# Kernel tuning notes

Hardware: AMD Instinct MI355X
Metric: run time of the kernel (lower is better)

The kernel has to match this reference:

```python
import jax, jax.numpy as jnp
import numpy as np

B, T, E, D, H = 8, 64, 4, 256, 1024  # batch, num_tokens, num_experts, hidden_dim, ffn_hidden_dim
SPARSITY_WEIGHT = 0.01


def setup_inputs() -> dict:
    key = jax.random.key(0)
    k_x, k_fc1, k_fc2, k_wr, k_br = jax.random.split(key, 5)
    x = jax.random.normal(k_x, (B, T, D), dtype=jnp.float32)
    # xavier_uniform per (t,e) slice: bound = sqrt(6/(fan_in+fan_out))
    a = float(np.sqrt(6.0 / (D + H)))
    fc1 = jax.random.uniform(k_fc1, (T, E, D, H), minval=-a, maxval=a, dtype=jnp.float32)
    b1 = jnp.zeros((T, E, H), dtype=jnp.float32)
    fc2 = jax.random.uniform(k_fc2, (T, E, H, D), minval=-a, maxval=a, dtype=jnp.float32)
    b2 = jnp.zeros((T, E, D), dtype=jnp.float32)
    # per-token routers (nn.Linear default init: U(-1/sqrt(D), 1/sqrt(D)))
    br_bound = float(1.0 / np.sqrt(D))
    Wr = jax.random.uniform(k_wr, (T, E, D), minval=-br_bound, maxval=br_bound, dtype=jnp.float32)
    br = jax.random.uniform(k_br, (T, E), minval=-br_bound, maxval=br_bound, dtype=jnp.float32)
    return {"x": x, "fc1": fc1, "b1": b1, "fc2": fc2, "b2": b2, "Wr": Wr, "br": br}


def reference(x, fc1, b1, fc2, b2, Wr, br):
    # x: [B,T,D]
    # ReLU routing gates per token/expert: [B,T,E]
    gates = jax.nn.relu(jnp.einsum('btd,ted->bte', x, Wr) + br)
    bsz = x.shape[0]
    aux_loss = SPARSITY_WEIGHT * gates.sum() / (bsz * x.shape[1])
    # Expert FFN, batched over (token, expert): hidden [B,T,E,H]
    hidden = jax.nn.gelu(jnp.einsum('btd,tedh->bteh', x, fc1) + b1, approximate=False)
    # dropout rate is 0.0 -> identity
    expert_out = jnp.einsum('bteh,tehd->bted', hidden, fc2) + b2  # [B,T,E,D]
    output = jnp.sum(expert_out * gates[..., None], axis=2)  # [B,T,D]
    return output, aux_loss
```

## Files before the change

kernel.cpp:

```cpp
#include <hip/hip_runtime.h>
#include <hip/hip_bf16.h>

namespace {

constexpr int kB = 8, kT = 64, kE = 4, kD = 256, kH = 1024;
constexpr int kNC = 4;
constexpr int kHc = kH / kNC;

__device__ __forceinline__ float gelu_exact(float v) {
  return 0.5f * v * (1.0f + erff(v * 0.70710678118654752f));
}

__global__ __launch_bounds__(256, 4)
void moe_ffn_kernel(const float* __restrict__ x,
                    const float* __restrict__ fc1,
                    const float* __restrict__ b1,
                    const float* __restrict__ fc2,
                    const float* __restrict__ b2,
                    const float* __restrict__ Wr,
                    const float* __restrict__ br,
                    float* __restrict__ out) {
  __shared__ float xs[kB][kD];
  __shared__ float hid[kB][kHc];
  __shared__ float gates_s[kB];

  const int tid = threadIdx.x;
  const int bid = blockIdx.x;
  const int te  = bid / kNC;
  const int c   = bid % kNC;
  const int t   = te >> 2;
  const int h0  = c * kHc;

#pragma unroll
  for (int b = 0; b < kB; ++b)
    xs[b][tid] = x[((size_t)b * kT + t) * kD + tid];
  __syncthreads();

  const int wave = tid >> 6, lane = tid & 63;

  {
    const float* __restrict__ wr = Wr + (size_t)te * kD;
    const float w0 = wr[lane], w1 = wr[lane + 64], w2 = wr[lane + 128], w3 = wr[lane + 192];
#pragma unroll
    for (int bb = 0; bb < 2; ++bb) {
      const int b = wave + bb * 4;
      float p = xs[b][lane] * w0 + xs[b][lane + 64] * w1 +
                xs[b][lane + 128] * w2 + xs[b][lane + 192] * w3;
#pragma unroll
      for (int off = 32; off; off >>= 1) p += __shfl_xor(p, off);
      if (lane == 0) {
        const float g = p + br[te];
        gates_s[b] = g > 0.0f ? g : 0.0f;
      }
    }
  }

  {
    const float* __restrict__ w = fc1 + (size_t)te * kD * kH + h0 + tid;
    float acc[kB] = {0.f, 0.f, 0.f, 0.f, 0.f, 0.f, 0.f, 0.f};
#pragma unroll 8
    for (int d = 0; d < kD; ++d) {
      const float wv = w[(size_t)d * kH];
#pragma unroll
      for (int b = 0; b < kB; ++b) acc[b] = fmaf(xs[b][d], wv, acc[b]);
    }
    const float bias = b1[(size_t)te * kH + h0 + tid];
#pragma unroll
    for (int b = 0; b < kB; ++b) hid[b][tid] = gelu_exact(acc[b] + bias);
  }
  __syncthreads();

  {
    const float* __restrict__ w = fc2 + (size_t)te * kH * kD + (size_t)h0 * kD + tid;
    float acc[kB] = {0.f, 0.f, 0.f, 0.f, 0.f, 0.f, 0.f, 0.f};
#pragma unroll 8
    for (int i = 0; i < kHc; ++i) {
      const float wv = w[(size_t)i * kD];
#pragma unroll
      for (int b = 0; b < kB; ++b) acc[b] = fmaf(hid[b][i], wv, acc[b]);
    }
    const float bias2 = (c == 0) ? b2[(size_t)te * kD + tid] : 0.f;
#pragma unroll
    for (int b = 0; b < kB; ++b)
      atomicAdd(&out[((size_t)b * kT + t) * kD + tid], gates_s[b] * (acc[b] + bias2));

    if (c == 0 && tid == 0) {
      float gs = 0.f;
#pragma unroll
      for (int b = 0; b < kB; ++b) gs += gates_s[b];
      atomicAdd(&out[(size_t)kB * kT * kD], 0.01f * gs * (1.0f / (kB * kT)));
    }
  }
}

}

extern "C" void kernel_launch(void* const* d_in, const int* in_sizes, int n_in,
                              void* d_out, int out_size, void* d_ws, size_t ws_size,
                              hipStream_t stream) {
  const float* x   = (const float*)d_in[0];
  const float* fc1 = (const float*)d_in[1];
  const float* b1  = (const float*)d_in[2];
  const float* fc2 = (const float*)d_in[3];
  const float* b2  = (const float*)d_in[4];
  const float* Wr  = (const float*)d_in[5];
  const float* br  = (const float*)d_in[6];
  float* out = (float*)d_out;

  hipMemsetAsync(d_out, 0, (size_t)out_size * sizeof(float), stream);

  moe_ffn_kernel<<<dim3(kT * kE * kNC), dim3(256), 0, stream>>>(x, fc1, b1, fc2, b2, Wr, br, out);
}
```

Baseline: 104.6 us.

## Split reduction dim across waves with float4 weight loads and LDS reduction

```diff
diff --git a/kernel.cpp b/kernel.cpp
--- a/kernel.cpp
+++ b/kernel.cpp
@@ -22,28 +22,35 @@
                     float* __restrict__ out) {
   __shared__ float xs[kB][kD];
   __shared__ float hid[kB][kHc];
+  __shared__ float red[kB][kD];
   __shared__ float gates_s[kB];
 
-  const int tid = threadIdx.x;
-  const int bid = blockIdx.x;
-  const int te  = bid / kNC;
-  const int c   = bid % kNC;
-  const int t   = te >> 2;
-  const int h0  = c * kHc;
-
-#pragma unroll
-  for (int b = 0; b < kB; ++b)
-    xs[b][tid] = x[((size_t)b * kT + t) * kD + tid];
+  const int tid  = threadIdx.x;
+  const int bid  = blockIdx.x;
+  const int te   = bid >> 2;
+  const int c    = bid & 3;
+  const int t    = te >> 2;
+  const int h0   = c * kHc;
+  const int wave = tid >> 6, lane = tid & 63;
+
+  {
+    const float4* __restrict__ xsrc = reinterpret_cast<const float4*>(x);
+    float4* xdst = reinterpret_cast<float4*>(&xs[0][0]);
+#pragma unroll
+    for (int i = 0; i < 2; ++i) {
+      const int f = i * 256 + tid;
+      const int b = f >> 6, d4 = f & 63;
+      xdst[f] = xsrc[(size_t)(b * kT + t) * (kD / 4) + d4];
+    }
+  }
   __syncthreads();
-
-  const int wave = tid >> 6, lane = tid & 63;
 
   {
     const float* __restrict__ wr = Wr + (size_t)te * kD;
     const float w0 = wr[lane], w1 = wr[lane + 64], w2 = wr[lane + 128], w3 = wr[lane + 192];
 #pragma unroll
     for (int bb = 0; bb < 2; ++bb) {
-      const int b = wave + bb * 4;
+      const int b = wave * 2 + bb;
       float p = xs[b][lane] * w0 + xs[b][lane + 64] * w1 +
                 xs[b][lane + 128] * w2 + xs[b][lane + 192] * w3;
 #pragma unroll
@@ -55,34 +62,125 @@
     }
   }
 
-  {
-    const float* __restrict__ w = fc1 + (size_t)te * kD * kH + h0 + tid;
-    float acc[kB] = {0.f, 0.f, 0.f, 0.f, 0.f, 0.f, 0.f, 0.f};
-#pragma unroll 8
-    for (int d = 0; d < kD; ++d) {
-      const float wv = w[(size_t)d * kH];
-#pragma unroll
-      for (int b = 0; b < kB; ++b) acc[b] = fmaf(xs[b][d], wv, acc[b]);
-    }
+  float4 acc[kB];
+#pragma unroll
+  for (int b = 0; b < kB; ++b) acc[b] = make_float4(0.f, 0.f, 0.f, 0.f);
+  {
+    const float4* __restrict__ wp =
+        reinterpret_cast<const float4*>(fc1 + (size_t)te * (kD * kH));
+    const int hq = (h0 >> 2) + lane;
+    const int d0 = wave * 64;
+    for (int dg = 0; dg < 16; ++dg) {
+      const int d = d0 + dg * 4;
+      const float4 wv0 = wp[(size_t)(d + 0) * (kH / 4) + hq];
+      const float4 wv1 = wp[(size_t)(d + 1) * (kH / 4) + hq];
+      const float4 wv2 = wp[(size_t)(d + 2) * (kH / 4) + hq];
+      const float4 wv3 = wp[(size_t)(d + 3) * (kH / 4) + hq];
+#pragma unroll
+      for (int b = 0; b < kB; ++b) {
+        const float4 xv = *reinterpret_cast<const float4*>(&xs[b][d]);
+        acc[b].x = fmaf(xv.x, wv0.x, acc[b].x);
+        acc[b].y = fmaf(xv.x, wv0.y, acc[b].y);
+        acc[b].z = fmaf(xv.x, wv0.z, acc[b].z);
+        acc[b].w = fmaf(xv.x, wv0.w, acc[b].w);
+        acc[b].x = fmaf(xv.y, wv1.x, acc[b].x);
+        acc[b].y = fmaf(xv.y, wv1.y, acc[b].y);
+        acc[b].z = fmaf(xv.y, wv1.z, acc[b].z);
+        acc[b].w = fmaf(xv.y, wv1.w, acc[b].w);
+        acc[b].x = fmaf(xv.z, wv2.x, acc[b].x);
+        acc[b].y = fmaf(xv.z, wv2.y, acc[b].y);
+        acc[b].z = fmaf(xv.z, wv2.z, acc[b].z);
+        acc[b].w = fmaf(xv.z, wv2.w, acc[b].w);
+        acc[b].x = fmaf(xv.w, wv3.x, acc[b].x);
+        acc[b].y = fmaf(xv.w, wv3.y, acc[b].y);
+        acc[b].z = fmaf(xv.w, wv3.z, acc[b].z);
+        acc[b].w = fmaf(xv.w, wv3.w, acc[b].w);
+      }
+    }
+  }
+#pragma unroll
+  for (int g = 0; g < 4; ++g) {
+    if (wave == g) {
+#pragma unroll
+      for (int b = 0; b < kB; ++b) {
+        float4* hp = reinterpret_cast<float4*>(&hid[b][0]) + lane;
+        if (g == 0) {
+          *hp = acc[b];
+        } else {
+          float4 v = *hp;
+          v.x += acc[b].x; v.y += acc[b].y; v.z += acc[b].z; v.w += acc[b].w;
+          *hp = v;
+        }
+      }
+    }
+    __syncthreads();
+  }
+  {
     const float bias = b1[(size_t)te * kH + h0 + tid];
 #pragma unroll
-    for (int b = 0; b < kB; ++b) hid[b][tid] = gelu_exact(acc[b] + bias);
+    for (int b = 0; b < kB; ++b) hid[b][tid] = gelu_exact(hid[b][tid] + bias);
   }
   __syncthreads();
 
-  {
-    const float* __restrict__ w = fc2 + (size_t)te * kH * kD + (size_t)h0 * kD + tid;
-    float acc[kB] = {0.f, 0.f, 0.f, 0.f, 0.f, 0.f, 0.f, 0.f};
-#pragma unroll 8
-    for (int i = 0; i < kHc; ++i) {
-      const float wv = w[(size_t)i * kD];
-#pragma unroll
-      for (int b = 0; b < kB; ++b) acc[b] = fmaf(hid[b][i], wv, acc[b]);
-    }
-    const float bias2 = (c == 0) ? b2[(size_t)te * kD + tid] : 0.f;
+  float4 acc2[kB];
+#pragma unroll
+  for (int b = 0; b < kB; ++b) acc2[b] = make_float4(0.f, 0.f, 0.f, 0.f);
+  {
+    const float4* __restrict__ wp =
+        reinterpret_cast<const float4*>(fc2 + (size_t)te * (kH * kD));
+    const int hb = wave * 64;
+    for (int hg = 0; hg < 16; ++hg) {
+      const int hl = hb + hg * 4;
+      const int h  = h0 + hl;
+      const float4 wv0 = wp[(size_t)(h + 0) * (kD / 4) + lane];
+      const float4 wv1 = wp[(size_t)(h + 1) * (kD / 4) + lane];
+      const float4 wv2 = wp[(size_t)(h + 2) * (kD / 4) + lane];
+      const float4 wv3 = wp[(size_t)(h + 3) * (kD / 4) + lane];
+#pragma unroll
+      for (int b = 0; b < kB; ++b) {
+        const float4 hv = *reinterpret_cast<const float4*>(&hid[b][hl]);
+        acc2[b].x = fmaf(hv.x, wv0.x, acc2[b].x);
+        acc2[b].y = fmaf(hv.x, wv0.y, acc2[b].y);
+        acc2[b].z = fmaf(hv.x, wv0.z, acc2[b].z);
+        acc2[b].w = fmaf(hv.x, wv0.w, acc2[b].w);
+        acc2[b].x = fmaf(hv.y, wv1.x, acc2[b].x);
+        acc2[b].y = fmaf(hv.y, wv1.y, acc2[b].y);
+        acc2[b].z = fmaf(hv.y, wv1.z, acc2[b].z);
+        acc2[b].w = fmaf(hv.y, wv1.w, acc2[b].w);
+        acc2[b].x = fmaf(hv.z, wv2.x, acc2[b].x);
+        acc2[b].y = fmaf(hv.z, wv2.y, acc2[b].y);
+        acc2[b].z = fmaf(hv.z, wv2.z, acc2[b].z);
+        acc2[b].w = fmaf(hv.z, wv2.w, acc2[b].w);
+        acc2[b].x = fmaf(hv.w, wv3.x, acc2[b].x);
+        acc2[b].y = fmaf(hv.w, wv3.y, acc2[b].y);
+        acc2[b].z = fmaf(hv.w, wv3.z, acc2[b].z);
+        acc2[b].w = fmaf(hv.w, wv3.w, acc2[b].w);
+      }
+    }
+  }
+#pragma unroll
+  for (int g = 0; g < 4; ++g) {
+    if (wave == g) {
+#pragma unroll
+      for (int b = 0; b < kB; ++b) {
+        float4* rp = reinterpret_cast<float4*>(&red[b][0]) + lane;
+        if (g == 0) {
+          *rp = acc2[b];
+        } else {
+          float4 v = *rp;
+          v.x += acc2[b].x; v.y += acc2[b].y; v.z += acc2[b].z; v.w += acc2[b].w;
+          *rp = v;
+        }
+      }
+    }
+    __syncthreads();
+  }
+
+  {
+    const float b2v = (c == 0) ? b2[(size_t)te * kD + tid] : 0.f;
 #pragma unroll
     for (int b = 0; b < kB; ++b)
-      atomicAdd(&out[((size_t)b * kT + t) * kD + tid], gates_s[b] * (acc[b] + bias2));
+      atomicAdd(&out[((size_t)b * kT + t) * kD + tid], gates_s[b] * (red[b][tid] + b2v));
 
     if (c == 0 && tid == 0) {
       float gs = 0.f;
@@ -109,5 +207,6 @@
 
   hipMemsetAsync(d_out, 0, (size_t)out_size * sizeof(float), stream);
 
-  moe_ffn_kernel<<<dim3(kT * kE * kNC), dim3(256), 0, stream>>>(x, fc1, b1, fc2, b2, Wr, br, out);
-}
+  moe_ffn_kernel<<<dim3(kT * kE * kNC), dim3(256), 0, stream>>>(
+      x, fc1, b1, fc2, b2, Wr, br, out);
+}
```

After: 107.2 us. 1.02x slower.

## Use one block per token-expert with float4 nontemporal weight loads and shuffled hidden

Applied to the files above, without the earlier changes.

```diff
diff --git a/kernel.cpp b/kernel.cpp
--- a/kernel.cpp
+++ b/kernel.cpp
@@ -4,14 +4,19 @@
 namespace {
 
 constexpr int kB = 8, kT = 64, kE = 4, kD = 256, kH = 1024;
-constexpr int kNC = 4;
-constexpr int kHc = kH / kNC;
+
+typedef float floatx4 __attribute__((ext_vector_type(4)));
 
 __device__ __forceinline__ float gelu_exact(float v) {
   return 0.5f * v * (1.0f + erff(v * 0.70710678118654752f));
 }
 
-__global__ __launch_bounds__(256, 4)
+__device__ __forceinline__ float4 ntload4(const float4* p) {
+  const floatx4 v = __builtin_nontemporal_load(reinterpret_cast<const floatx4*>(p));
+  return make_float4(v.x, v.y, v.z, v.w);
+}
+
+__global__ __launch_bounds__(256, 1)
 void moe_ffn_kernel(const float* __restrict__ x,
                     const float* __restrict__ fc1,
                     const float* __restrict__ b1,
@@ -21,73 +26,144 @@
                     const float* __restrict__ br,
                     float* __restrict__ out) {
   __shared__ float xs[kB][kD];
-  __shared__ float hid[kB][kHc];
-  __shared__ float gates_s[kB];
 
-  const int tid = threadIdx.x;
-  const int bid = blockIdx.x;
-  const int te  = bid / kNC;
-  const int c   = bid % kNC;
-  const int t   = te >> 2;
-  const int h0  = c * kHc;
+  const int tid  = threadIdx.x;
+  const int te   = blockIdx.x;
+  const int t    = te >> 2;
+  const int wave = tid >> 6, lane = tid & 63;
+  const int c    = wave;
 
+  {
+    const float4* __restrict__ xsrc = reinterpret_cast<const float4*>(x);
+    float4* xdst = reinterpret_cast<float4*>(&xs[0][0]);
 #pragma unroll
-  for (int b = 0; b < kB; ++b)
-    xs[b][tid] = x[((size_t)b * kT + t) * kD + tid];
+    for (int i = 0; i < 2; ++i) {
+      const int f = i * 256 + tid;
+      const int b = f >> 6, d4 = f & 63;
+      xdst[f] = xsrc[(size_t)(b * kT + t) * (kD / 4) + d4];
+    }
+  }
   __syncthreads();
 
-  const int wave = tid >> 6, lane = tid & 63;
-
+  float gates[kB];
   {
     const float* __restrict__ wr = Wr + (size_t)te * kD;
     const float w0 = wr[lane], w1 = wr[lane + 64], w2 = wr[lane + 128], w3 = wr[lane + 192];
+    const float brv = br[te];
 #pragma unroll
-    for (int bb = 0; bb < 2; ++bb) {
-      const int b = wave + bb * 4;
+    for (int b = 0; b < kB; ++b) {
       float p = xs[b][lane] * w0 + xs[b][lane + 64] * w1 +
                 xs[b][lane + 128] * w2 + xs[b][lane + 192] * w3;
 #pragma unroll
       for (int off = 32; off; off >>= 1) p += __shfl_xor(p, off);
-      if (lane == 0) {
-        const float g = p + br[te];
-        gates_s[b] = g > 0.0f ? g : 0.0f;
+      const float g = p + brv;
+      gates[b] = g > 0.0f ? g : 0.0f;
+    }
+  }
+
+  float4 hid[kB];
+  {
+    float4 a[kB];
+#pragma unroll
+    for (int b = 0; b < kB; ++b) a[b] = make_float4(0.f, 0.f, 0.f, 0.f);
+    const float4* __restrict__ wp =
+        reinterpret_cast<const float4*>(fc1 + (size_t)te * (kD * kH));
+    const int hq = c * 64 + lane;
+#pragma unroll 2
+    for (int dg = 0; dg < 64; ++dg) {
+      const int d = dg * 4;
+      const float4 wv0 = ntload4(wp + (size_t)(d + 0) * (kH / 4) + hq);
+      const float4 wv1 = ntload4(wp + (size_t)(d + 1) * (kH / 4) + hq);
+      const float4 wv2 = ntload4(wp + (size_t)(d + 2) * (kH / 4) + hq);
+      const float4 wv3 = ntload4(wp + (size_t)(d + 3) * (kH / 4) + hq);
+#pragma unroll
+      for (int b = 0; b < kB; ++b) {
+        const float4 xv = *reinterpret_cast<const float4*>(&xs[b][d]);
+        a[b].x = fmaf(xv.x, wv0.x, a[b].x);
+        a[b].y = fmaf(xv.x, wv0.y, a[b].y);
+        a[b].z = fmaf(xv.x, wv0.z, a[b].z);
+        a[b].w = fmaf(xv.x, wv0.w, a[b].w);
+        a[b].x = fmaf(xv.y, wv1.x, a[b].x);
+        a[b].y = fmaf(xv.y, wv1.y, a[b].y);
+        a[b].z = fmaf(xv.y, wv1.z, a[b].z);
+        a[b].w = fmaf(xv.y, wv1.w, a[b].w);
+        a[b].x = fmaf(xv.z, wv2.x, a[b].x);
+        a[b].y = fmaf(xv.z, wv2.y, a[b].y);
+        a[b].z = fmaf(xv.z, wv2.z, a[b].z);
+        a[b].w = fmaf(xv.z, wv2.w, a[b].w);
+        a[b].x = fmaf(xv.w, wv3.x, a[b].x);
+        a[b].y = fmaf(xv.w, wv3.y, a[b].y);
+        a[b].z = fmaf(xv.w, wv3.z, a[b].z);
+        a[b].w = fmaf(xv.w, wv3.w, a[b].w);
+      }
+    }
+    const float4 bias =
+        *reinterpret_cast<const float4*>(&b1[(size_t)te * kH + c * 256 + 4 * lane]);
+#pragma unroll
+    for (int b = 0; b < kB; ++b) {
+      hid[b].x = gelu_exact(a[b].x + bias.x);
+      hid[b].y = gelu_exact(a[b].y + bias.y);
+      hid[b].z = gelu_exact(a[b].z + bias.z);
+      hid[b].w = gelu_exact(a[b].w + bias.w);
+    }
+  }
+
+  float4 acc2[kB];
+#pragma unroll
+  for (int b = 0; b < kB; ++b) acc2[b] = make_float4(0.f, 0.f, 0.f, 0.f);
+  {
+    const float4* __restrict__ wp2 =
+        reinterpret_cast<const float4*>(fc2 + (size_t)te * (kH * kD)) + lane;
+#pragma unroll 2
+    for (int hg = 0; hg < 64; ++hg) {
+      const int hrow = c * 256 + hg * 4;
+      const float4 wv0 = ntload4(wp2 + (size_t)(hrow + 0) * (kD / 4));
+      const float4 wv1 = ntload4(wp2 + (size_t)(hrow + 1) * (kD / 4));
+      const float4 wv2 = ntload4(wp2 + (size_t)(hrow + 2) * (kD / 4));
+      const float4 wv3 = ntload4(wp2 + (size_t)(hrow + 3) * (kD / 4));
+#pragma unroll
+      for (int b = 0; b < kB; ++b) {
+        const float hx = __shfl(hid[b].x, hg);
+        const float hy = __shfl(hid[b].y, hg);
+        const float hz = __shfl(hid[b].z, hg);
+        const float hw = __shfl(hid[b].w, hg);
+        acc2[b].x = fmaf(hx, wv0.x, acc2[b].x);
+        acc2[b].y = fmaf(hx, wv0.y, acc2[b].y);
+        acc2[b].z = fmaf(hx, wv0.z, acc2[b].z);
+        acc2[b].w = fmaf(hx, wv0.w, acc2[b].w);
+        acc2[b].x = fmaf(hy, wv1.x, acc2[b].x);
+        acc2[b].y = fmaf(hy, wv1.y, acc2[b].y);
+        acc2[b].z = fmaf(hy, wv1.z, acc2[b].z);
+        acc2[b].w = fmaf(hy, wv1.w, acc2[b].w);
+        acc2[b].x = fmaf(hz, wv2.x, acc2[b].x);
+        acc2[b].y = fmaf(hz, wv2.y, acc2[b].y);
+        acc2[b].z = fmaf(hz, wv2.z, acc2[b].z);
+        acc2[b].w = fmaf(hz, wv2.w, acc2[b].w);
+        acc2[b].x = fmaf(hw, wv3.x, acc2[b].x);
+        acc2[b].y = fmaf(hw, wv3.y, acc2[b].y);
+        acc2[b].z = fmaf(hw, wv3.z, acc2[b].z);
+        acc2[b].w = fmaf(hw, wv3.w, acc2[b].w);
       }
     }
   }
 
   {
-    const float* __restrict__ w = fc1 + (size_t)te * kD * kH + h0 + tid;
-    float acc[kB] = {0.f, 0.f, 0.f, 0.f, 0.f, 0.f, 0.f, 0.f};
-#pragma unroll 8
-    for (int d = 0; d < kD; ++d) {
-      const float wv = w[(size_t)d * kH];
+    const int d0 = 4 * lane;
+    float4 b2v = make_float4(0.f, 0.f, 0.f, 0.f);
+    if (wave == 0) b2v = *reinterpret_cast<const float4*>(&b2[(size_t)te * kD + d0]);
 #pragma unroll
-      for (int b = 0; b < kB; ++b) acc[b] = fmaf(xs[b][d], wv, acc[b]);
+    for (int b = 0; b < kB; ++b) {
+      const float g = gates[b];
+      float* o = &out[((size_t)b * kT + t) * kD + d0];
+      atomicAdd(o + 0, g * (acc2[b].x + b2v.x));
+      atomicAdd(o + 1, g * (acc2[b].y + b2v.y));
+      atomicAdd(o + 2, g * (acc2[b].z + b2v.z));
+      atomicAdd(o + 3, g * (acc2[b].w + b2v.w));
     }
-    const float bias = b1[(size_t)te * kH + h0 + tid];
-#pragma unroll
-    for (int b = 0; b < kB; ++b) hid[b][tid] = gelu_exact(acc[b] + bias);
-  }
-  __syncthreads();
-
-  {
-    const float* __restrict__ w = fc2 + (size_t)te * kH * kD + (size_t)h0 * kD + tid;
-    float acc[kB] = {0.f, 0.f, 0.f, 0.f, 0.f, 0.f, 0.f, 0.f};
-#pragma unroll 8
-    for (int i = 0; i < kHc; ++i) {
-      const float wv = w[(size_t)i * kD];
-#pragma unroll
-      for (int b = 0; b < kB; ++b) acc[b] = fmaf(hid[b][i], wv, acc[b]);
-    }
-    const float bias2 = (c == 0) ? b2[(size_t)te * kD + tid] : 0.f;
-#pragma unroll
-    for (int b = 0; b < kB; ++b)
-      atomicAdd(&out[((size_t)b * kT + t) * kD + tid], gates_s[b] * (acc[b] + bias2));
-
-    if (c == 0 && tid == 0) {
+    if (wave == 0 && lane == 0) {
       float gs = 0.f;
 #pragma unroll
-      for (int b = 0; b < kB; ++b) gs += gates_s[b];
+      for (int b = 0; b < kB; ++b) gs += gates[b];
       atomicAdd(&out[(size_t)kB * kT * kD], 0.01f * gs * (1.0f / (kB * kT)));
     }
   }
@@ -107,7 +183,8 @@
   const float* br  = (const float*)d_in[6];
   float* out = (float*)d_out;
 
-  hipMemsetAsync(d_out, 0, (size_t)out_size * sizeof(float), stream);
+  (void)hipMemsetAsync(d_out, 0, (size_t)out_size * sizeof(float), stream);
 
-  moe_ffn_kernel<<<dim3(kT * kE * kNC), dim3(256), 0, stream>>>(x, fc1, b1, fc2, b2, Wr, br, out);
+  moe_ffn_kernel<<<dim3(kT * kE), dim3(256), 0, stream>>>(
+      x, fc1, b1, fc2, b2, Wr, br, out);
 }
```

After: 156.7 us. 49.8% more time.
